# Kernel optimization log

Hardware: AMD Instinct MI355X
Metric: run time of the kernel (lower is better)

## Reference

```python
import jax, jax.numpy as jnp
import numpy as np

N = 262144          # batch size
C = 100             # num_classes
R0, R1 = 0.95, 1.0  # recall_range
LAM = 0.5           # lambda_pauc
LS = 0.1            # label_smoothing
MAX_PAUC = R1 - R0


def setup_inputs() -> dict:
    key = jax.random.key(0)
    k1, k2 = jax.random.split(key)
    predictions = jax.random.normal(k1, (N, C), dtype=jnp.float32)
    targets = jax.random.randint(k2, (N,), 0, C)
    weight = jnp.ones((C,), dtype=jnp.float32)
    return {"predictions": predictions, "targets": targets, "weight": weight}


def _roc_curves(scores, labels):
    """Vectorized per-class ROC. scores, labels: [C, N].
    Replaces the O(N^2) per-threshold loop with sort + cumsum (tie-correct:
    tp at threshold s_j counts ALL samples with score >= s_j)."""
    order = jnp.argsort(-scores, axis=1)                      # descending
    ss = jnp.take_along_axis(scores, order, axis=1)           # [C, N]
    sl = jnp.take_along_axis(labels, order, axis=1)           # [C, N]
    cpos = jnp.cumsum(sl, axis=1)                             # cumulative positives
    # last index within each tie-group of equal scores
    neg = -ss  # ascending
    idx = jax.vmap(lambda a: jnp.searchsorted(a, a, side='right'))(neg) - 1
    tp = jnp.take_along_axis(cpos, idx, axis=1)
    cnt = (idx + 1).astype(scores.dtype)
    fp = cnt - tp
    P = cpos[:, -1:]                       # total positives per class
    Nn = scores.shape[1] - P               # total negatives per class
    tpr = jnp.where(P > 0, tp / jnp.maximum(P, 1.0), 0.0)
    fpr = jnp.where(Nn > 0, fp / jnp.maximum(Nn, 1.0), 0.0)
    return fpr, tpr


def reference(predictions, targets, weight):
    probs = jax.nn.softmax(predictions, axis=1)               # [N, C]
    onehot = jnp.eye(C, dtype=predictions.dtype)[targets]     # [N, C]
    onehot_s = (1.0 - LS) * onehot + LS / C

    # per-class binary labels (smoothed true-class value > 0.5)
    labels = (onehot_s > 0.5).astype(predictions.dtype).T     # [C, N]
    scores = probs.T                                          # [C, N]

    fpr, tpr = _roc_curves(scores, labels)
    mask = (tpr >= R0) & (tpr <= R1)
    y = jnp.maximum(tpr - R0, 0.0)
    # tpr is monotone non-decreasing, so the recall mask is contiguous and
    # trapz over the masked subset == sum over adjacent pairs both in mask.
    pm = (mask[:, :-1] & mask[:, 1:]).astype(predictions.dtype)
    pauc = jnp.sum(0.5 * (y[:, :-1] + y[:, 1:]) * (fpr[:, 1:] - fpr[:, :-1]) * pm, axis=1)  # [C]

    avg_p_auc = jnp.sum(pauc * weight) / (jnp.sum(weight) * MAX_PAUC)
    # torch computes TP/FP via .item(): the pAUC path carries no gradient
    avg_p_auc = jax.lax.stop_gradient(jnp.clip(avg_p_auc, 0.0, 1.0))

    log_probs = jax.nn.log_softmax(predictions, axis=1)
    ce_loss = -jnp.mean(jnp.sum(onehot_s * log_probs * weight, axis=1))
    pauc_loss = 1.0 - avg_p_auc ** 2
    return (1.0 - LAM) * ce_loss + LAM * pauc_loss
```

## Files before the change

### kernel.cpp

```cpp
#include <hip/hip_runtime.h>
#include <math.h>

#define WAVE 64
constexpr int   CC      = 100;
constexpr int   MAXM    = 160;
constexpr int   BUCKET  = 4096;
constexpr int   USTRIDE = 161;
constexpr int   LCAP    = 2048;
constexpr float LSMOOTH = 0.1f;
constexpr int   TILE    = 64;
constexpr int   T4TILE  = TILE * CC / 4;
constexpr int   K3AGRID = 1024;
constexpr int   K3BGRID = 512;

__device__ __forceinline__ void gload_lds16(const void* g, void* lds) {
    __builtin_amdgcn_global_load_lds(
        (const __attribute__((address_space(1))) void*)g,
        (__attribute__((address_space(3))) void*)lds, 16, 0, 0);
}

__global__ __launch_bounds__(256) void k1_tile(
    const float* __restrict__ pred, const int* __restrict__ targets,
    const float* __restrict__ weight, float* __restrict__ L_out,
    float* __restrict__ pos_out, float* __restrict__ ce_partial, int N)
{
    __shared__ float tile[TILE * CC];
    __shared__ int   ttgt[TILE];
    __shared__ float tL[TILE], tpos[TILE];
    __shared__ float cered[4];
    const int tid = threadIdx.x;
    const int r0  = blockIdx.x * TILE;

    const float4* src = (const float4*)(pred + (size_t)r0 * CC);
    {
        int t = tid;
        #pragma unroll
        for (int k = 0; k < T4TILE / 256; ++k) {
            gload_lds16((const void*)(src + t), (char*)tile + (size_t)t * 16);
            t += 256;
        }
        if (t < T4TILE)
            gload_lds16((const void*)(src + t), (char*)tile + (size_t)t * 16);
    }
    if (tid < TILE) ttgt[tid] = targets[r0 + tid];
    asm volatile("s_waitcnt vmcnt(0)" ::: "memory");
    __syncthreads();

    const int x = tid & 15;
    const int G = tid >> 4;
    float w[7];
    #pragma unroll
    for (int j = 0; j < 7; ++j) {
        int c = x + 16 * j;
        w[j] = (c < CC) ? weight[c] : 0.0f;
    }
    float Wl = 0.0f;
    #pragma unroll
    for (int j = 0; j < 7; ++j) Wl += w[j];
    #pragma unroll
    for (int off = 1; off < 16; off <<= 1) Wl += __shfl_xor(Wl, off, 16);

    float ce_acc = 0.0f;
    #pragma unroll
    for (int rr = 0; rr < 4; ++rr) {
        const int r = G * 4 + rr;
        const float* rp = tile + r * CC;
        float v[7];
        #pragma unroll
        for (int j = 0; j < 7; ++j) {
            int c = x + 16 * j;
            v[j] = (c < CC) ? rp[c] : -INFINITY;
        }
        float vmax = v[0];
        #pragma unroll
        for (int j = 1; j < 7; ++j) vmax = fmaxf(vmax, v[j]);
        #pragma unroll
        for (int off = 1; off < 16; off <<= 1) vmax = fmaxf(vmax, __shfl_xor(vmax, off, 16));
        float z = 0.0f, ws = 0.0f;
        #pragma unroll
        for (int j = 0; j < 7; ++j) {
            int c = x + 16 * j;
            if (c < CC) { z += __expf(v[j] - vmax); ws += w[j] * v[j]; }
        }
        #pragma unroll
        for (int off = 1; off < 16; off <<= 1) {
            z  += __shfl_xor(z,  off, 16);
            ws += __shfl_xor(ws, off, 16);
        }
        float L = vmax + __logf(z);
        if (x == 0) {
            int t = ttgt[r];
            float pt = rp[t];
            tL[r] = L; tpos[r] = pt - L;
            ce_acc += -((1.0f - LSMOOTH) * weight[t] * (pt - L)
                        + (LSMOOTH / CC) * (ws - Wl * L));
        }
    }
    #pragma unroll
    for (int off = 32; off; off >>= 1) ce_acc += __shfl_xor(ce_acc, off, WAVE);
    if ((tid & 63) == 0) cered[tid >> 6] = ce_acc;
    __syncthreads();
    if (tid < TILE) {
        L_out[r0 + tid]   = tL[tid];
        pos_out[r0 + tid] = tpos[tid];
    }
    if (tid == 0)
        ce_partial[blockIdx.x] = cered[0] + cered[1] + cered[2] + cered[3];
}

__global__ __launch_bounds__(256) void k1b_scatter(
    const int* __restrict__ targets, const float* __restrict__ pos,
    int* __restrict__ cls_cnt, float* __restrict__ bucket, int N)
{
    __shared__ int hist[CC];
    __shared__ int base[CC];
    __shared__ int loc[CC];
    const int tid = threadIdx.x;
    const int rowsPerBlock = N / gridDim.x;
    const int r0 = blockIdx.x * rowsPerBlock;
    const int r1 = r0 + rowsPerBlock;
    for (int c = tid; c < CC; c += blockDim.x) { hist[c] = 0; loc[c] = 0; }
    __syncthreads();
    for (int r = r0 + tid; r < r1; r += blockDim.x)
        atomicAdd(&hist[targets[r]], 1);
    __syncthreads();
    for (int c = tid; c < CC; c += blockDim.x)
        base[c] = (hist[c] > 0) ? atomicAdd(&cls_cnt[c], hist[c]) : 0;
    __syncthreads();
    for (int r = r0 + tid; r < r1; r += blockDim.x) {
        int c = targets[r];
        int idx = base[c] + atomicAdd(&loc[c], 1);
        if (idx < BUCKET) bucket[(size_t)c * BUCKET + idx] = pos[r];
    }
}

__global__ __launch_bounds__(256) void k2_select(
    const float* __restrict__ bucket, const int* __restrict__ cls_cnt,
    float* __restrict__ u, int* __restrict__ m_arr, int* __restrict__ P_arr,
    float* __restrict__ wm_arr)
{
    __shared__ unsigned int keys[BUCKET];
    __shared__ unsigned int hist[256];
    __shared__ unsigned int scan[256];
    __shared__ unsigned int sel[256];
    __shared__ unsigned int s_prefix;
    __shared__ int s_rank;
    __shared__ int cnt_lt;
    const int c   = blockIdx.x;
    const int tid = threadIdx.x;
    const int P = min(cls_cnt[c], BUCKET);
    double Kd = 0.95 * (double)P;
    int kf = (int)floor(Kd);
    int m = P - kf;
    if (m > MAXM) m = MAXM;
    if (m < 0) m = 0;
    if (tid == 0) {
        m_arr[c] = m; P_arr[c] = P;
        wm_arr[c] = (float)((double)(kf + 1) - Kd);
        s_prefix = 0; s_rank = m - 1; cnt_lt = 0;
    }
    for (int i = tid; i < P; i += 256) {
        unsigned int b = __float_as_uint(bucket[(size_t)c * BUCKET + i]);
        keys[i] = (b & 0x80000000u) ? ~b : (b | 0x80000000u);
    }
    __syncthreads();
    if (m == 0) return;

    for (int shift = 24; shift >= 0; shift -= 8) {
        hist[tid] = 0;
        __syncthreads();
        unsigned int pref = s_prefix;
        for (int i = tid; i < P; i += 256) {
            unsigned int k = keys[i];
            bool match = (shift == 24) || ((k >> (shift + 8)) == pref);
            if (match) atomicAdd(&hist[(k >> shift) & 255u], 1u);
        }
        __syncthreads();
        if (tid < 64) {
            unsigned h0 = hist[tid*4], h1 = hist[tid*4+1],
                     h2 = hist[tid*4+2], h3 = hist[tid*4+3];
            unsigned s0 = h0, s1 = s0 + h1, s2 = s1 + h2, s3 = s2 + h3;
            unsigned sc = s3;
            #pragma unroll
            for (int off = 1; off < 64; off <<= 1) {
                unsigned t2 = __shfl_up(sc, (unsigned)off, 64);
                if (tid >= off) sc += t2;
            }
            unsigned excl = sc - s3;
            scan[tid*4]   = excl + s0;
            scan[tid*4+1] = excl + s1;
            scan[tid*4+2] = excl + s2;
            scan[tid*4+3] = excl + s3;
        }
        __syncthreads();
        int r = s_rank;
        unsigned int inc = scan[tid];
        unsigned int exc = inc - hist[tid];
        __syncthreads();
        if ((unsigned int)r >= exc && (unsigned int)r < inc) {
            s_rank   = r - (int)exc;
            s_prefix = (pref << 8) | (unsigned int)tid;
        }
        __syncthreads();
    }
    const unsigned int kth = s_prefix;

    for (int i = tid; i < P; i += 256) {
        unsigned int k = keys[i];
        if (k < kth) {
            int pslot = atomicAdd(&cnt_lt, 1);
            sel[pslot] = k;
        }
    }
    __syncthreads();
    const int nlt = cnt_lt;
    for (int j = nlt + tid; j < 256; j += 256) sel[j] = (j < m) ? kth : 0xFFFFFFFFu;
    __syncthreads();
    for (int kk = 2; kk <= 256; kk <<= 1) {
        for (int j = kk >> 1; j > 0; j >>= 1) {
            int i = tid, ixj = tid ^ j;
            if (ixj > i) {
                unsigned int a = sel[i], b = sel[ixj];
                bool up = ((i & kk) == 0);
                if ((a > b) == up) { sel[i] = b; sel[ixj] = a; }
            }
            __syncthreads();
        }
    }
    if (tid < m) {
        unsigned int k = sel[tid];
        unsigned int b = (k & 0x80000000u) ? (k & 0x7fffffffu) : ~k;
        u[c * MAXM + tid] = __uint_as_float(b);
    }
}

__device__ __forceinline__ int ubound(const float* uc, int m, float key, int maxidx) {
    int l = 0;
    #pragma unroll
    for (int s = 128; s; s >>= 1) {
        int p = l + s - 1;
        float val = uc[p < maxidx ? p : maxidx];
        l += ((p < m) && (val <= key)) ? s : 0;
    }
    return l;
}

__global__ __launch_bounds__(256) void k3a_stream(
    const float4* __restrict__ pred4, const float* __restrict__ L,
    const float* __restrict__ u, const int* __restrict__ m_arr,
    uint2* __restrict__ list, int* __restrict__ list_cnt, int list_cap,
    int* __restrict__ g_cnt, int* __restrict__ g_sum, int total4)
{
    __shared__ float umax_s[CC];
    __shared__ uint2 buf[LCAP];
    __shared__ int lcnt;
    __shared__ int gbase;
    const int tid = threadIdx.x;
    if (tid < CC) {
        int m = m_arr[tid];
        umax_s[tid] = (m > 0) ? u[tid * MAXM + m - 1] : -INFINITY;
    }
    if (tid == 0) lcnt = 0;
    __syncthreads();

    auto proc = [&](float4 v, float Ln, int j) {
        float4 um = *((const float4*)&umax_s[j * 4]);
        float s0 = v.x - Ln, s1 = v.y - Ln, s2 = v.z - Ln, s3 = v.w - Ln;
        #pragma unroll
        for (int q = 0; q < 4; ++q) {
            float scv = (q == 0) ? s0 : (q == 1) ? s1 : (q == 2) ? s2 : s3;
            float mx  = (q == 0) ? um.x : (q == 1) ? um.y : (q == 2) ? um.z : um.w;
            if (scv < mx) {
                int c = j * 4 + q;
                int idx = atomicAdd(&lcnt, 1);
                if (idx < LCAP) {
                    buf[idx] = make_uint2((unsigned int)c, __float_as_uint(scv));
                } else {
                    int m = m_arr[c];
                    int l = ubound(u + c * MAXM, m, scv, MAXM - 1);
                    atomicAdd(&g_cnt[c], 1);
                    atomicAdd(&g_sum[c], m - 1 - l);
                }
            }
        }
    };

    const int stride = K3AGRID * 256;
    int i = blockIdx.x * 256 + tid;
    while (i < total4) {
        int i2 = i + stride;
        bool has2 = (i2 < total4);
        float4 v0 = pred4[i];
        float4 v1 = has2 ? pred4[i2] : make_float4(0.f, 0.f, 0.f, 0.f);
        int n0 = i / 25, j0 = i - n0 * 25;
        float L0 = L[n0];
        proc(v0, L0, j0);
        if (has2) {
            int n1 = i2 / 25, j1 = i2 - n1 * 25;
            proc(v1, L[n1], j1);
        }
        i += 2 * stride;
    }
    __syncthreads();
    int cnt = min(lcnt, LCAP);
    if (tid == 0) gbase = atomicAdd(list_cnt, cnt);
    __syncthreads();
    const int base0 = gbase;
    for (int k = tid; k < cnt; k += 256) {
        int gi = base0 + k;
        if (gi < list_cap) {
            list[gi] = buf[k];
        } else {
            uint2 e = buf[k];
            int c = (int)e.x; float scv = __uint_as_float(e.y);
            int m = m_arr[c];
            int l = ubound(u + c * MAXM, m, scv, MAXM - 1);
            atomicAdd(&g_cnt[c], 1);
            atomicAdd(&g_sum[c], m - 1 - l);
        }
    }
}

__global__ __launch_bounds__(256) void k3b_rank_final(
    const uint2* __restrict__ list, const int* __restrict__ list_cnt, int list_cap,
    const float* __restrict__ u, const int* __restrict__ m_arr,
    const int* __restrict__ P_arr, const float* __restrict__ wm_arr,
    const float* __restrict__ weight, const float* __restrict__ ce_partial,
    int nPartial, int* __restrict__ g_cnt, int* __restrict__ g_sum,
    int* __restrict__ done, float* __restrict__ out, int N)
{
    __shared__ float us[CC * USTRIDE];
    __shared__ int sm[CC], lcnt[CC], lsum[CC];
    __shared__ int lastflag;
    __shared__ double r1[256], r2[256], r3[256];
    const int tid = threadIdx.x;
    for (int c = tid; c < CC; c += 256) { sm[c] = m_arr[c]; lcnt[c] = 0; lsum[c] = 0; }
    for (int t = tid; t < CC * MAXM; t += 256) {
        int c = t / MAXM, k = t - c * MAXM;
        us[c * USTRIDE + k] = u[t];
    }
    __syncthreads();
    const int n = min(*list_cnt, list_cap);
    const int stride = K3BGRID * 256;
    for (int base = blockIdx.x * 256 + tid; base < n; base += 4 * stride) {
        int  cc4[4]; int mm4[4]; float kk4[4]; bool hh4[4];
        #pragma unroll
        for (int t = 0; t < 4; ++t) {
            int idx = base + t * stride;
            bool h = idx < n;
            uint2 e = h ? list[idx] : make_uint2(0u, 0u);
            hh4[t] = h;
            cc4[t] = (int)e.x;
            mm4[t] = h ? sm[(int)e.x] : 0;
            kk4[t] = __uint_as_float(e.y);
        }
        int ll4[4] = {0, 0, 0, 0};
        #pragma unroll
        for (int s = 128; s; s >>= 1) {
            #pragma unroll
            for (int t = 0; t < 4; ++t) {
                int p = ll4[t] + s - 1;
                float val = us[cc4[t] * USTRIDE + (p < USTRIDE - 1 ? p : USTRIDE - 1)];
                ll4[t] += ((p < mm4[t]) && (val <= kk4[t])) ? s : 0;
            }
        }
        #pragma unroll
        for (int t = 0; t < 4; ++t)
            if (hh4[t]) {
                atomicAdd(&lcnt[cc4[t]], 1);
                atomicAdd(&lsum[cc4[t]], mm4[t] - 1 - ll4[t]);
            }
    }
    __syncthreads();
    for (int c = tid; c < CC; c += 256)
        if (lcnt[c]) { atomicAdd(&g_cnt[c], lcnt[c]); atomicAdd(&g_sum[c], lsum[c]); }
    __threadfence();
    __syncthreads();
    if (tid == 0) {
        int r = atomicAdd(done, 1);
        lastflag = (r == (int)gridDim.x - 1) ? 1 : 0;
    }
    __syncthreads();
    if (!lastflag) return;

    double ce = 0.0;
    for (int t = tid; t < nPartial; t += 256) ce += (double)ce_partial[t];
    double p = 0.0, wsum = 0.0;
    for (int c = tid; c < CC; c += 256) {
        int P = P_arr[c], m = m_arr[c];
        double wgt = (double)weight[c];
        long long Nn = (long long)N - P;
        if (P > 0 && Nn > 0 && m > 0) {
            int gc = __hip_atomic_load(&g_cnt[c], __ATOMIC_RELAXED, __HIP_MEMORY_SCOPE_AGENT);
            int gs = __hip_atomic_load(&g_sum[c], __ATOMIC_RELAXED, __HIP_MEMORY_SCOPE_AGENT);
            double wm = (double)wm_arr[c];
            double S   = (double)gs + wm * (double)gc;
            double sub = 0.5 * (double)(m - 1) * (double)(m - 2) + wm * (double)(m - 1);
            double pc  = (S - sub) / ((double)Nn * (double)P);
            if (pc < 0.0) pc = 0.0;
            p += pc * wgt;
        }
        wsum += wgt;
    }
    r1[tid] = ce; r2[tid] = p; r3[tid] = wsum;
    __syncthreads();
    for (int off = 128; off; off >>= 1) {
        if (tid < off) {
            r1[tid] += r1[tid + off];
            r2[tid] += r2[tid + off];
            r3[tid] += r3[tid + off];
        }
        __syncthreads();
    }
    if (tid == 0) {
        double ce_loss = r1[0] / (double)N;
        double avg = r2[0] / (r3[0] * 0.05);
        avg = fmin(fmax(avg, 0.0), 1.0);
        out[0] = (float)(0.5 * ce_loss + 0.5 * (1.0 - avg * avg));
    }
}

extern "C" void kernel_launch(void* const* d_in, const int* in_sizes, int n_in,
                              void* d_out, int out_size, void* d_ws, size_t ws_size,
                              hipStream_t stream) {
    (void)n_in; (void)out_size;
    const float* pred    = (const float*)d_in[0];
    const int*   targets = (const int*)d_in[1];
    const float* weight  = (const float*)d_in[2];
    float* out = (float*)d_out;
    const int N = in_sizes[1];

    const int K1_BLOCKS = N / TILE;
    char* base = (char*)d_ws;
    size_t off = 0;
    auto take = [&](size_t bytes) { char* q = base + off; off += (bytes + 15) & ~(size_t)15; return q; };
    float* L_ws       = (float*)take((size_t)N * 4);
    float* pos_ws     = (float*)take((size_t)N * 4);
    float* ce_partial = (float*)take((size_t)K1_BLOCKS * 4);
    float* u          = (float*)take((size_t)CC * MAXM * 4);
    int*   m_arr      = (int*)take(CC * 4);
    int*   P_arr      = (int*)take(CC * 4);
    float* wm_arr     = (float*)take(CC * 4);
    int*   zero_blk   = (int*)take(304 * 4);
    int*   cls_cnt  = zero_blk;
    int*   g_cnt    = zero_blk + CC;
    int*   g_sum    = zero_blk + 2 * CC;
    int*   list_cnt = zero_blk + 3 * CC;
    int*   done     = zero_blk + 3 * CC + 1;
    float* bucket     = (float*)take((size_t)CC * BUCKET * 4);
    uint2* list       = (uint2*)(base + off);
    long long rem     = (long long)ws_size - (long long)off;
    int list_cap      = (rem > 0) ? (int)(rem / 8) : 0;

    hipMemsetAsync(zero_blk, 0, 304 * 4, stream);

    k1_tile<<<K1_BLOCKS, 256, 0, stream>>>(pred, targets, weight, L_ws, pos_ws,
                                           ce_partial, N);
    k1b_scatter<<<256, 256, 0, stream>>>(targets, pos_ws, cls_cnt, bucket, N);
    k2_select<<<CC, 256, 0, stream>>>(bucket, cls_cnt, u, m_arr, P_arr, wm_arr);
    const int total4 = (int)((size_t)N * CC / 4);
    k3a_stream<<<K3AGRID, 256, 0, stream>>>((const float4*)pred, L_ws, u, m_arr,
                                            list, list_cnt, list_cap, g_cnt, g_sum, total4);
    k3b_rank_final<<<K3BGRID, 256, 0, stream>>>(list, list_cnt, list_cap, u, m_arr,
                                                P_arr, wm_arr, weight, ce_partial,
                                                K1_BLOCKS, g_cnt, g_sum, done, out, N);
}
```

Measured before the change: 271.0 us.

## Split rank kernel from final reduction, widen ILP, pack LDS counters

The rank-counting kernel now processes eight list entries per thread instead of four, giving more independent binary searches over LDS to hide latency. Per-class count and sum are packed into one 64-bit LDS atomic instead of two 32-bit atomics. The last-block-done final reduction is moved into a separate single-block kernel, which removes the threadfence and the global done counter but adds one more launch. The 8-way unroll raises register pressure, and the packed sum relies on the low 32-bit field not carrying into the count.

```diff
diff --git a/kernel.cpp b/kernel.cpp
--- a/kernel.cpp
+++ b/kernel.cpp
@@ -321,20 +321,16 @@
     }
 }
 
-__global__ __launch_bounds__(256) void k3b_rank_final(
+__global__ __launch_bounds__(256) void k3b_rank(
     const uint2* __restrict__ list, const int* __restrict__ list_cnt, int list_cap,
     const float* __restrict__ u, const int* __restrict__ m_arr,
-    const int* __restrict__ P_arr, const float* __restrict__ wm_arr,
-    const float* __restrict__ weight, const float* __restrict__ ce_partial,
-    int nPartial, int* __restrict__ g_cnt, int* __restrict__ g_sum,
-    int* __restrict__ done, float* __restrict__ out, int N)
+    int* __restrict__ g_cnt, int* __restrict__ g_sum)
 {
     __shared__ float us[CC * USTRIDE];
-    __shared__ int sm[CC], lcnt[CC], lsum[CC];
-    __shared__ int lastflag;
-    __shared__ double r1[256], r2[256], r3[256];
+    __shared__ int sm[CC];
+    __shared__ unsigned long long lpack[CC];
     const int tid = threadIdx.x;
-    for (int c = tid; c < CC; c += 256) { sm[c] = m_arr[c]; lcnt[c] = 0; lsum[c] = 0; }
+    for (int c = tid; c < CC; c += 256) { sm[c] = m_arr[c]; lpack[c] = 0ull; }
     for (int t = tid; t < CC * MAXM; t += 256) {
         int c = t / MAXM, k = t - c * MAXM;
         us[c * USTRIDE + k] = u[t];
@@ -342,59 +338,64 @@
     __syncthreads();
     const int n = min(*list_cnt, list_cap);
     const int stride = K3BGRID * 256;
-    for (int base = blockIdx.x * 256 + tid; base < n; base += 4 * stride) {
-        int  cc4[4]; int mm4[4]; float kk4[4]; bool hh4[4];
-        #pragma unroll
-        for (int t = 0; t < 4; ++t) {
+    for (int base = blockIdx.x * 256 + tid; base < n; base += 8 * stride) {
+        int bb8[8]; int mm8[8]; float kk8[8]; bool hh8[8]; int cc8[8];
+        #pragma unroll
+        for (int t = 0; t < 8; ++t) {
             int idx = base + t * stride;
             bool h = idx < n;
             uint2 e = h ? list[idx] : make_uint2(0u, 0u);
-            hh4[t] = h;
-            cc4[t] = (int)e.x;
-            mm4[t] = h ? sm[(int)e.x] : 0;
-            kk4[t] = __uint_as_float(e.y);
-        }
-        int ll4[4] = {0, 0, 0, 0};
+            hh8[t] = h;
+            cc8[t] = (int)e.x;
+            bb8[t] = (int)e.x * USTRIDE;
+            mm8[t] = h ? sm[(int)e.x] : 0;
+            kk8[t] = __uint_as_float(e.y);
+        }
+        int ll8[8] = {0, 0, 0, 0, 0, 0, 0, 0};
         #pragma unroll
         for (int s = 128; s; s >>= 1) {
             #pragma unroll
-            for (int t = 0; t < 4; ++t) {
-                int p = ll4[t] + s - 1;
-                float val = us[cc4[t] * USTRIDE + (p < USTRIDE - 1 ? p : USTRIDE - 1)];
-                ll4[t] += ((p < mm4[t]) && (val <= kk4[t])) ? s : 0;
+            for (int t = 0; t < 8; ++t) {
+                int p = ll8[t] + s - 1;
+                float val = us[bb8[t] + (p < USTRIDE - 1 ? p : USTRIDE - 1)];
+                ll8[t] += ((p < mm8[t]) && (val <= kk8[t])) ? s : 0;
             }
         }
         #pragma unroll
-        for (int t = 0; t < 4; ++t)
-            if (hh4[t]) {
-                atomicAdd(&lcnt[cc4[t]], 1);
-                atomicAdd(&lsum[cc4[t]], mm4[t] - 1 - ll4[t]);
+        for (int t = 0; t < 8; ++t)
+            if (hh8[t]) {
+                unsigned long long pk =
+                    (1ull << 32) | (unsigned long long)(unsigned)(mm8[t] - 1 - ll8[t]);
+                atomicAdd(&lpack[cc8[t]], pk);
             }
     }
     __syncthreads();
-    for (int c = tid; c < CC; c += 256)
-        if (lcnt[c]) { atomicAdd(&g_cnt[c], lcnt[c]); atomicAdd(&g_sum[c], lsum[c]); }
-    __threadfence();
-    __syncthreads();
-    if (tid == 0) {
-        int r = atomicAdd(done, 1);
-        lastflag = (r == (int)gridDim.x - 1) ? 1 : 0;
-    }
-    __syncthreads();
-    if (!lastflag) return;
-
+    for (int c = tid; c < CC; c += 256) {
+        unsigned long long pk = lpack[c];
+        int cnt = (int)(pk >> 32);
+        int sum = (int)(pk & 0xffffffffull);
+        if (cnt) { atomicAdd(&g_cnt[c], cnt); atomicAdd(&g_sum[c], sum); }
+    }
+}
+
+__global__ __launch_bounds__(256) void k4_final(
+    const float* __restrict__ ce_partial, int nPartial,
+    const float* __restrict__ weight, const int* __restrict__ P_arr,
+    const int* __restrict__ m_arr, const float* __restrict__ wm_arr,
+    const int* __restrict__ g_cnt, const int* __restrict__ g_sum,
+    float* __restrict__ out, int N)
+{
+    __shared__ double r1[256], r2[256], r3[256];
     double ce = 0.0;
-    for (int t = tid; t < nPartial; t += 256) ce += (double)ce_partial[t];
+    for (int i = threadIdx.x; i < nPartial; i += blockDim.x) ce += (double)ce_partial[i];
     double p = 0.0, wsum = 0.0;
-    for (int c = tid; c < CC; c += 256) {
+    for (int c = threadIdx.x; c < CC; c += blockDim.x) {
         int P = P_arr[c], m = m_arr[c];
         double wgt = (double)weight[c];
         long long Nn = (long long)N - P;
         if (P > 0 && Nn > 0 && m > 0) {
-            int gc = __hip_atomic_load(&g_cnt[c], __ATOMIC_RELAXED, __HIP_MEMORY_SCOPE_AGENT);
-            int gs = __hip_atomic_load(&g_sum[c], __ATOMIC_RELAXED, __HIP_MEMORY_SCOPE_AGENT);
             double wm = (double)wm_arr[c];
-            double S   = (double)gs + wm * (double)gc;
+            double S   = (double)g_sum[c] + wm * (double)g_cnt[c];
             double sub = 0.5 * (double)(m - 1) * (double)(m - 2) + wm * (double)(m - 1);
             double pc  = (S - sub) / ((double)Nn * (double)P);
             if (pc < 0.0) pc = 0.0;
@@ -402,17 +403,17 @@
         }
         wsum += wgt;
     }
-    r1[tid] = ce; r2[tid] = p; r3[tid] = wsum;
-    __syncthreads();
-    for (int off = 128; off; off >>= 1) {
-        if (tid < off) {
-            r1[tid] += r1[tid + off];
-            r2[tid] += r2[tid + off];
-            r3[tid] += r3[tid + off];
-        }
-        __syncthreads();
-    }
-    if (tid == 0) {
+    r1[threadIdx.x] = ce; r2[threadIdx.x] = p; r3[threadIdx.x] = wsum;
+    __syncthreads();
+    for (int off = blockDim.x >> 1; off; off >>= 1) {
+        if ((int)threadIdx.x < off) {
+            r1[threadIdx.x] += r1[threadIdx.x + off];
+            r2[threadIdx.x] += r2[threadIdx.x + off];
+            r3[threadIdx.x] += r3[threadIdx.x + off];
+        }
+        __syncthreads();
+    }
+    if (threadIdx.x == 0) {
         double ce_loss = r1[0] / (double)N;
         double avg = r2[0] / (r3[0] * 0.05);
         avg = fmin(fmax(avg, 0.0), 1.0);
@@ -446,7 +447,6 @@
     int*   g_cnt    = zero_blk + CC;
     int*   g_sum    = zero_blk + 2 * CC;
     int*   list_cnt = zero_blk + 3 * CC;
-    int*   done     = zero_blk + 3 * CC + 1;
     float* bucket     = (float*)take((size_t)CC * BUCKET * 4);
     uint2* list       = (uint2*)(base + off);
     long long rem     = (long long)ws_size - (long long)off;
@@ -461,7 +461,8 @@
     const int total4 = (int)((size_t)N * CC / 4);
     k3a_stream<<<K3AGRID, 256, 0, stream>>>((const float4*)pred, L_ws, u, m_arr,
                                             list, list_cnt, list_cap, g_cnt, g_sum, total4);
-    k3b_rank_final<<<K3BGRID, 256, 0, stream>>>(list, list_cnt, list_cap, u, m_arr,
-                                                P_arr, wm_arr, weight, ce_partial,
-                                                K1_BLOCKS, g_cnt, g_sum, done, out, N);
-}
+    k3b_rank<<<K3BGRID, 256, 0, stream>>>(list, list_cnt, list_cap, u, m_arr,
+                                          g_cnt, g_sum);
+    k4_final<<<1, 256, 0, stream>>>(ce_partial, K1_BLOCKS, weight, P_arr, m_arr, wm_arr,
+                                    g_cnt, g_sum, out, N);
+}
```

Measured after the change: 254.4 us. 1.07x faster.
